# Performance work log

Measured on AMD Instinct MI355X. Metric: run time of the kernel, lower is better.

The kernel has to match this reference:

```python
import jax, jax.numpy as jnp
import numpy as np

B, C, H, W = 8192, 3, 32, 32
IN_FEATURES = C * H * W  # 3072, hardcoded in the module


def setup_inputs() -> dict:
    key = jax.random.key(0)
    k1, k2 = jax.random.split(key)
    x = jax.random.normal(k1, (B, C, H, W), dtype=jnp.float32)
    noise = jax.random.normal(k2, (B, C, H, W), dtype=jnp.float32)  # randn_like(x)
    logvar_t = jnp.array([-1.0], dtype=jnp.float32)  # nn.Parameter init
    return {"x": x, "noise": noise, "logvar_t": logvar_t}


def reference(x, noise, logvar_t):
    # additive branch of view_learner.forward
    n_batch = x.shape[0]
    x_t = x + jnp.exp(0.5 * logvar_t[0]) * noise
    var = jnp.exp(logvar_t[0]) + 1e-10
    xf = x.reshape(n_batch, IN_FEATURES)
    # compute_distances: x_norm + x_t_norm - 2 * x @ x.T, clamped to [0, inf)
    x_norm = jnp.sum(xf * xf, axis=1)  # [B]
    dist = x_norm[:, None] + x_norm[None, :] - 2.0 * (xf @ xf.T)  # [B, B]
    dist = jnp.maximum(dist, 0.0)
    distance_contribution = -jnp.mean(jax.nn.logsumexp(-0.5 * dist / var, axis=1))
    normalization_constant = jnp.log(jnp.float32(n_batch))
    kl_xt = (normalization_constant + distance_contribution) / jnp.log(jnp.float32(2.0))
    return x_t, kl_xt
```

## Files before the change

### kernel.cpp

```cpp
#include <hip/hip_runtime.h>
#include <cstdint>

#define K_DIM 3072
#define B_DIM 8192
#define ROW_B 3072
#define ROW_U 768
#define BMA   256
#define BNB   128
#define NTB   64
#define NKT   48

typedef __attribute__((ext_vector_type(4))) float        f32x4;
typedef __attribute__((ext_vector_type(4))) int          i32x4;

#define QS     16.0f
#define INV_S2 0.00390625f

__device__ __forceinline__ int q8(float f) {
    int q = __float2int_rn(f * QS);
    return max(-127, min(127, q));
}
__device__ __forceinline__ unsigned pack4(float a, float b, float c, float d) {
    return (unsigned)(q8(a) & 0xFF)
         | ((unsigned)(q8(b) & 0xFF) << 8)
         | ((unsigned)(q8(c) & 0xFF) << 16)
         | ((unsigned)(q8(d) & 0xFF) << 24);
}

__global__ __launch_bounds__(384) void prep_kernel(const float* __restrict__ x,
                                                   const float* __restrict__ nz,
                                                   const float* __restrict__ logvar,
                                                   float* __restrict__ xt,
                                                   unsigned int* __restrict__ xb,
                                                   float* __restrict__ xn,
                                                   float* __restrict__ se)
{
    const int row = blockIdx.x;
    const int tid = threadIdx.x;
    const float4* xr = (const float4*)(x + (size_t)row * K_DIM);
    float4 v0 = xr[2 * tid];
    float4 v1 = xr[2 * tid + 1];
    float s = v0.x * v0.x + v0.y * v0.y + v0.z * v0.z + v0.w * v0.w
            + v1.x * v1.x + v1.y * v1.y + v1.z * v1.z + v1.w * v1.w;

    if (xt) {
        const float4* nr = (const float4*)(nz + (size_t)row * K_DIM);
        float4 n0 = nr[2 * tid], n1 = nr[2 * tid + 1];
        const float sc = __expf(0.5f * logvar[0]);
        float4 o0, o1;
        o0.x = fmaf(sc, n0.x, v0.x); o0.y = fmaf(sc, n0.y, v0.y);
        o0.z = fmaf(sc, n0.z, v0.z); o0.w = fmaf(sc, n0.w, v0.w);
        o1.x = fmaf(sc, n1.x, v1.x); o1.y = fmaf(sc, n1.y, v1.y);
        o1.z = fmaf(sc, n1.z, v1.z); o1.w = fmaf(sc, n1.w, v1.w);
        float4* tr = (float4*)(xt + (size_t)row * K_DIM);
        tr[2 * tid] = o0;
        tr[2 * tid + 1] = o1;
    }

    unsigned int* dst = xb + (size_t)row * ROW_U + tid * 2;
    dst[0] = pack4(v0.x, v0.y, v0.z, v0.w);
    dst[1] = pack4(v1.x, v1.y, v1.z, v1.w);

#pragma unroll
    for (int d = 32; d > 0; d >>= 1) s += __shfl_down(s, d);
    __shared__ float red[6];
    if ((tid & 63) == 0) red[tid >> 6] = s;
    __syncthreads();
    if (tid == 0) {
        float t = 0.f;
#pragma unroll
        for (int i = 0; i < 6; ++i) t += red[i];
        xn[row] = t;
        se[row] = 0.f;
    }
}

__global__ __launch_bounds__(512, 4) void gram_lse_kernel(const unsigned int* __restrict__ xb,
                                                          const float* __restrict__ xn,
                                                          const float* __restrict__ logvar,
                                                          float* __restrict__ se)
{
    __shared__ __align__(1024) unsigned char lds[3][24576];

    int rem = blockIdx.x;
    int a = 0;
    while (rem >= NTB - 2 * a) { rem -= NTB - 2 * a; ++a; }
    const int v = 2 * a + rem;

    const int tid  = threadIdx.x;
    const int lane = tid & 63;
    const int wave = tid >> 6;
    const int wr = wave >> 1, wc = wave & 1;
    const int fc = lane >> 4;

    const size_t rowA0 = (size_t)a * BMA;
    const size_t rowB0 = (size_t)v * BNB;
    const unsigned char* xb8 = (const unsigned char*)xb;

    unsigned int srcOff[3];
    int dstOff[3];
#pragma unroll
    for (int l = 0; l < 3; ++l) {
        const int e = (l < 2) ? (l * 512 + tid) : tid;
        const int r = e >> 2, c = e & 3;
        const int csw = c ^ ((r >> 1) & 3);
        const size_t rb = ((l < 2) ? rowA0 : rowB0) + (size_t)r;
        srcOff[l] = (unsigned int)(rb * ROW_B + (size_t)csw * 16);
        dstOff[l] = ((l < 2) ? 0 : 16384) + e * 16;
    }

    i32x4 acc[4][4];
#pragma unroll
    for (int i = 0; i < 4; ++i)
#pragma unroll
        for (int j = 0; j < 4; ++j) acc[i][j] = (i32x4){0, 0, 0, 0};

#pragma unroll
    for (int l = 0; l < 3; ++l)
        __builtin_amdgcn_global_load_lds(
            (const __attribute__((address_space(1))) void*)(xb8 + srcOff[l]),
            (__attribute__((address_space(3))) void*)(&lds[0][0] + dstOff[l]), 16, 0, 0);
#pragma unroll
    for (int l = 0; l < 3; ++l)
        __builtin_amdgcn_global_load_lds(
            (const __attribute__((address_space(1))) void*)(xb8 + srcOff[l] + 64u),
            (__attribute__((address_space(3))) void*)(&lds[1][0] + dstOff[l]), 16, 0, 0);
    asm volatile("s_waitcnt vmcnt(3)" ::: "memory");
    asm volatile("s_barrier" ::: "memory");

    for (int t = 0; t < NKT; ++t) {
        const unsigned char* cur = &lds[t % 3][0];

        if (t + 2 < NKT) {
            unsigned char* nxt = &lds[(t + 2) % 3][0];
            const unsigned int kg = (unsigned int)(t + 2) * 64u;
#pragma unroll
            for (int l = 0; l < 3; ++l)
                __builtin_amdgcn_global_load_lds(
                    (const __attribute__((address_space(1))) void*)(xb8 + srcOff[l] + kg),
                    (__attribute__((address_space(3))) void*)(nxt + dstOff[l]), 16, 0, 0);
        }

        i32x4 aF[4], bF[4];
#pragma unroll
        for (int mi = 0; mi < 4; ++mi) {
            const int r = wr * 64 + mi * 16 + (lane & 15);
            const int phys = fc ^ ((r >> 1) & 3);
            aF[mi] = *(const i32x4*)(cur + r * 64 + phys * 16);
        }
#pragma unroll
        for (int ni = 0; ni < 4; ++ni) {
            const int r = wc * 64 + ni * 16 + (lane & 15);
            const int phys = fc ^ ((r >> 1) & 3);
            bF[ni] = *(const i32x4*)(cur + 16384 + r * 64 + phys * 16);
        }

        __builtin_amdgcn_s_setprio(1);
#pragma unroll
        for (int mi = 0; mi < 4; ++mi)
#pragma unroll
            for (int ni = 0; ni < 4; ++ni)
                acc[mi][ni] = __builtin_amdgcn_mfma_i32_16x16x64_i8(
                    aF[mi], bF[ni], acc[mi][ni], 0, 0, 0);
        __builtin_amdgcn_s_setprio(0);

        if (t + 2 < NKT)
            asm volatile("s_waitcnt vmcnt(3)" ::: "memory");
        else
            asm volatile("s_waitcnt vmcnt(0)" ::: "memory");
        asm volatile("s_barrier" ::: "memory");
    }

    const float lv  = logvar[0];
    const float var = __expf(lv) + 1e-10f;
    const float cc  = 0.5f / var;

    const int u = 2 * a + (wr >> 1);
    if (u > v) return;

    const int colBase = (int)rowB0 + wc * 64 + (lane & 15);
    const int rowBase = (int)rowA0 + wr * 64 + (lane >> 4) * 4;

#pragma unroll
    for (int mi = 0; mi < 4; ++mi) {
#pragma unroll
        for (int rg = 0; rg < 4; ++rg) {
            const int i = rowBase + mi * 16 + rg;
            const float xni = xn[i];
            float rs = 0.f;
#pragma unroll
            for (int ni = 0; ni < 4; ++ni) {
                const int j = colBase + ni * 16;
                const float g = (float)acc[mi][ni][rg] * INV_S2;
                const float dist = xni + xn[j] - 2.f * g;
                rs += (i == j) ? 1.0f : __expf(-cc * fmaxf(dist, 0.f));
            }
#pragma unroll
            for (int d = 1; d < 16; d <<= 1) rs += __shfl_xor(rs, d);
            if ((lane & 15) == 0) atomicAdd(&se[i], rs);
        }
    }

    if (u < v) {
#pragma unroll
        for (int ni = 0; ni < 4; ++ni) {
            const int j = colBase + ni * 16;
            const float xnj = xn[j];
            float cs = 0.f;
#pragma unroll
            for (int mi = 0; mi < 4; ++mi)
#pragma unroll
                for (int rg = 0; rg < 4; ++rg) {
                    const int i = rowBase + mi * 16 + rg;
                    const float g = (float)acc[mi][ni][rg] * INV_S2;
                    cs += __expf(-cc * fmaxf(xn[i] + xnj - 2.f * g, 0.f));
                }
#pragma unroll
            for (int d = 16; d < 64; d <<= 1) cs += __shfl_xor(cs, d);
            if ((lane >> 4) == 0) atomicAdd(&se[j], cs);
        }
    }
}

__global__ __launch_bounds__(256) void kl_kernel(const float* __restrict__ se,
                                                 float* __restrict__ out)
{
    const int tid = threadIdx.x;
    float s = 0.f;
    for (int i = tid; i < B_DIM; i += 256) s += logf(se[i]);
#pragma unroll
    for (int d = 32; d > 0; d >>= 1) s += __shfl_down(s, d);
    __shared__ float red[4];
    if ((tid & 63) == 0) red[tid >> 6] = s;
    __syncthreads();
    if (tid == 0) {
        const float dc = -(red[0] + red[1] + red[2] + red[3]) / (float)B_DIM;
        out[0] = (logf((float)B_DIM) + dc) / logf(2.f);
    }
}

__global__ __launch_bounds__(256) void xt_kernel(const float4* __restrict__ x,
                                                 const float4* __restrict__ nz,
                                                 const float* __restrict__ logvar,
                                                 float4* __restrict__ out, int n4)
{
    const float sc = expf(0.5f * logvar[0]);
    for (int i = blockIdx.x * blockDim.x + threadIdx.x; i < n4;
         i += gridDim.x * blockDim.x) {
        float4 va = x[i], vb = nz[i];
        float4 o;
        o.x = fmaf(sc, vb.x, va.x);
        o.y = fmaf(sc, vb.y, va.y);
        o.z = fmaf(sc, vb.z, va.z);
        o.w = fmaf(sc, vb.w, va.w);
        out[i] = o;
    }
}

extern "C" void kernel_launch(void* const* d_in, const int* in_sizes, int n_in,
                              void* d_out, int out_size, void* d_ws, size_t ws_size,
                              hipStream_t stream)
{
    const float* x      = (const float*)d_in[0];
    const float* noise  = (const float*)d_in[1];
    const float* logvar = (const float*)d_in[2];
    float* out = (float*)d_out;

    const size_t NEL      = (size_t)B_DIM * K_DIM;
    const size_t XB_BYTES = (size_t)B_DIM * ROW_B;
    const size_t NTILES   = 1056;

    const bool use_ws = ws_size >= XB_BYTES + 2 * (size_t)B_DIM * sizeof(float) + 256;

    if (use_ws) {
        unsigned int* xb = (unsigned int*)d_ws;
        float* xn = (float*)((char*)d_ws + XB_BYTES);
        float* se = xn + B_DIM;

        prep_kernel<<<B_DIM, 384, 0, stream>>>(x, noise, logvar, out, xb, xn, se);
        gram_lse_kernel<<<(int)NTILES, 512, 0, stream>>>(xb, xn, logvar, se);
        kl_kernel<<<1, 256, 0, stream>>>(se, out + NEL);
    } else {
        unsigned int* xb = (unsigned int*)d_out;
        float* xn = (float*)((char*)d_out + (32u << 20));
        float* se = xn + B_DIM;

        prep_kernel<<<B_DIM, 384, 0, stream>>>(x, noise, logvar, nullptr, xb, xn, se);
        gram_lse_kernel<<<(int)NTILES, 512, 0, stream>>>(xb, xn, logvar, se);
        kl_kernel<<<1, 256, 0, stream>>>(se, out + NEL);
        xt_kernel<<<2048, 256, 0, stream>>>((const float4*)x, (const float4*)noise,
                                            logvar, (float4*)out, (int)(NEL / 4));
    }
}
```

Before: 210.3 us.

## Use square 128x128 triangular tiles and double-buffer register fragments across k-steps

```diff
diff --git a/kernel.cpp b/kernel.cpp
--- a/kernel.cpp
+++ b/kernel.cpp
@@ -5,13 +5,12 @@
 #define B_DIM 8192
 #define ROW_B 3072
 #define ROW_U 768
-#define BMA   256
-#define BNB   128
-#define NTB   64
+#define BT    128
+#define NTT   64
 #define NKT   48
 
-typedef __attribute__((ext_vector_type(4))) float        f32x4;
-typedef __attribute__((ext_vector_type(4))) int          i32x4;
+typedef __attribute__((ext_vector_type(4))) float f32x4;
+typedef __attribute__((ext_vector_type(4))) int   i32x4;
 
 #define QS     16.0f
 #define INV_S2 0.00390625f
@@ -75,17 +74,19 @@
     }
 }
 
-__global__ __launch_bounds__(512, 4) void gram_lse_kernel(const unsigned int* __restrict__ xb,
+struct Frags { i32x4 a[4]; i32x4 b[4]; };
+
+__global__ __launch_bounds__(256, 3) void gram_lse_kernel(const unsigned int* __restrict__ xb,
                                                           const float* __restrict__ xn,
                                                           const float* __restrict__ logvar,
                                                           float* __restrict__ se)
 {
-    __shared__ __align__(1024) unsigned char lds[3][24576];
+    __shared__ __align__(1024) unsigned char lds[3][16384];
 
     int rem = blockIdx.x;
-    int a = 0;
-    while (rem >= NTB - 2 * a) { rem -= NTB - 2 * a; ++a; }
-    const int v = 2 * a + rem;
+    int bm = 0;
+    while (rem >= NTT - bm) { rem -= NTT - bm; ++bm; }
+    const int bn = bm + rem;
 
     const int tid  = threadIdx.x;
     const int lane = tid & 63;
@@ -93,20 +94,20 @@
     const int wr = wave >> 1, wc = wave & 1;
     const int fc = lane >> 4;
 
-    const size_t rowA0 = (size_t)a * BMA;
-    const size_t rowB0 = (size_t)v * BNB;
+    const size_t rowA0 = (size_t)bm * BT;
+    const size_t rowB0 = (size_t)bn * BT;
     const unsigned char* xb8 = (const unsigned char*)xb;
 
-    unsigned int srcOff[3];
-    int dstOff[3];
-#pragma unroll
-    for (int l = 0; l < 3; ++l) {
-        const int e = (l < 2) ? (l * 512 + tid) : tid;
+    unsigned int srcOff[4];
+    int dstOff[4];
+#pragma unroll
+    for (int l = 0; l < 4; ++l) {
+        const int e = (l & 1) * 256 + tid;
         const int r = e >> 2, c = e & 3;
         const int csw = c ^ ((r >> 1) & 3);
         const size_t rb = ((l < 2) ? rowA0 : rowB0) + (size_t)r;
         srcOff[l] = (unsigned int)(rb * ROW_B + (size_t)csw * 16);
-        dstOff[l] = ((l < 2) ? 0 : 16384) + e * 16;
+        dstOff[l] = ((l < 2) ? 0 : 8192) + e * 16;
     }
 
     i32x4 acc[4][4];
@@ -115,68 +116,78 @@
 #pragma unroll
         for (int j = 0; j < 4; ++j) acc[i][j] = (i32x4){0, 0, 0, 0};
 
-#pragma unroll
-    for (int l = 0; l < 3; ++l)
+    int aOff[4], bOff[4];
+#pragma unroll
+    for (int mi = 0; mi < 4; ++mi) {
+        const int r = wr * 64 + mi * 16 + (lane & 15);
+        aOff[mi] = r * 64 + (fc ^ ((r >> 1) & 3)) * 16;
+    }
+#pragma unroll
+    for (int ni = 0; ni < 4; ++ni) {
+        const int r = wc * 64 + ni * 16 + (lane & 15);
+        bOff[ni] = 8192 + r * 64 + (fc ^ ((r >> 1) & 3)) * 16;
+    }
+
+#pragma unroll
+    for (int l = 0; l < 4; ++l)
         __builtin_amdgcn_global_load_lds(
             (const __attribute__((address_space(1))) void*)(xb8 + srcOff[l]),
             (__attribute__((address_space(3))) void*)(&lds[0][0] + dstOff[l]), 16, 0, 0);
 #pragma unroll
-    for (int l = 0; l < 3; ++l)
+    for (int l = 0; l < 4; ++l)
         __builtin_amdgcn_global_load_lds(
             (const __attribute__((address_space(1))) void*)(xb8 + srcOff[l] + 64u),
             (__attribute__((address_space(3))) void*)(&lds[1][0] + dstOff[l]), 16, 0, 0);
-    asm volatile("s_waitcnt vmcnt(3)" ::: "memory");
+    asm volatile("s_waitcnt vmcnt(4)" ::: "memory");
     asm volatile("s_barrier" ::: "memory");
 
-    for (int t = 0; t < NKT; ++t) {
-        const unsigned char* cur = &lds[t % 3][0];
-
+    Frags fA, fB;
+#pragma unroll
+    for (int mi = 0; mi < 4; ++mi) fA.a[mi] = *(const i32x4*)(&lds[0][0] + aOff[mi]);
+#pragma unroll
+    for (int ni = 0; ni < 4; ++ni) fA.b[ni] = *(const i32x4*)(&lds[0][0] + bOff[ni]);
+
+    auto body = [&](int t, Frags& cur, Frags& nxt) {
         if (t + 2 < NKT) {
-            unsigned char* nxt = &lds[(t + 2) % 3][0];
+            unsigned char* buf = &lds[(t + 2) % 3][0];
             const unsigned int kg = (unsigned int)(t + 2) * 64u;
 #pragma unroll
-            for (int l = 0; l < 3; ++l)
+            for (int l = 0; l < 4; ++l)
                 __builtin_amdgcn_global_load_lds(
                     (const __attribute__((address_space(1))) void*)(xb8 + srcOff[l] + kg),
-                    (__attribute__((address_space(3))) void*)(nxt + dstOff[l]), 16, 0, 0);
+                    (__attribute__((address_space(3))) void*)(buf + dstOff[l]), 16, 0, 0);
         }
-
-        i32x4 aF[4], bF[4];
-#pragma unroll
-        for (int mi = 0; mi < 4; ++mi) {
-            const int r = wr * 64 + mi * 16 + (lane & 15);
-            const int phys = fc ^ ((r >> 1) & 3);
-            aF[mi] = *(const i32x4*)(cur + r * 64 + phys * 16);
-        }
-#pragma unroll
-        for (int ni = 0; ni < 4; ++ni) {
-            const int r = wc * 64 + ni * 16 + (lane & 15);
-            const int phys = fc ^ ((r >> 1) & 3);
-            bF[ni] = *(const i32x4*)(cur + 16384 + r * 64 + phys * 16);
-        }
-
-        __builtin_amdgcn_s_setprio(1);
-#pragma unroll
-        for (int mi = 0; mi < 4; ++mi)
-#pragma unroll
-            for (int ni = 0; ni < 4; ++ni)
-                acc[mi][ni] = __builtin_amdgcn_mfma_i32_16x16x64_i8(
-                    aF[mi], bF[ni], acc[mi][ni], 0, 0, 0);
-        __builtin_amdgcn_s_setprio(0);
-
+        asm volatile("s_waitcnt lgkmcnt(0)" ::: "memory");
         if (t + 2 < NKT)
-            asm volatile("s_waitcnt vmcnt(3)" ::: "memory");
+            asm volatile("s_waitcnt vmcnt(4)" ::: "memory");
         else
             asm volatile("s_waitcnt vmcnt(0)" ::: "memory");
         asm volatile("s_barrier" ::: "memory");
+        if (t + 1 < NKT) {
+            const unsigned char* buf = &lds[(t + 1) % 3][0];
+#pragma unroll
+            for (int mi = 0; mi < 4; ++mi) nxt.a[mi] = *(const i32x4*)(buf + aOff[mi]);
+#pragma unroll
+            for (int ni = 0; ni < 4; ++ni) nxt.b[ni] = *(const i32x4*)(buf + bOff[ni]);
+        }
+        __builtin_amdgcn_s_setprio(1);
+#pragma unroll
+        for (int mi = 0; mi < 4; ++mi)
+#pragma unroll
+            for (int ni = 0; ni < 4; ++ni)
+                acc[mi][ni] = __builtin_amdgcn_mfma_i32_16x16x64_i8(
+                    cur.a[mi], cur.b[ni], acc[mi][ni], 0, 0, 0);
+        __builtin_amdgcn_s_setprio(0);
+    };
+
+    for (int tt = 0; tt < NKT / 2; ++tt) {
+        body(2 * tt,     fA, fB);
+        body(2 * tt + 1, fB, fA);
     }
 
     const float lv  = logvar[0];
     const float var = __expf(lv) + 1e-10f;
     const float cc  = 0.5f / var;
-
-    const int u = 2 * a + (wr >> 1);
-    if (u > v) return;
 
     const int colBase = (int)rowB0 + wc * 64 + (lane & 15);
     const int rowBase = (int)rowA0 + wr * 64 + (lane >> 4) * 4;
@@ -201,7 +212,7 @@
         }
     }
 
-    if (u < v) {
+    if (bm != bn) {
 #pragma unroll
         for (int ni = 0; ni < 4; ++ni) {
             const int j = colBase + ni * 16;
@@ -268,7 +279,7 @@
 
     const size_t NEL      = (size_t)B_DIM * K_DIM;
     const size_t XB_BYTES = (size_t)B_DIM * ROW_B;
-    const size_t NTILES   = 1056;
+    const int    NTILES   = NTT * (NTT + 1) / 2;
 
     const bool use_ws = ws_size >= XB_BYTES + 2 * (size_t)B_DIM * sizeof(float) + 256;
 
@@ -278,7 +289,7 @@
         float* se = xn + B_DIM;
 
         prep_kernel<<<B_DIM, 384, 0, stream>>>(x, noise, logvar, out, xb, xn, se);
-        gram_lse_kernel<<<(int)NTILES, 512, 0, stream>>>(xb, xn, logvar, se);
+        gram_lse_kernel<<<NTILES, 256, 0, stream>>>(xb, xn, logvar, se);
         kl_kernel<<<1, 256, 0, stream>>>(se, out + NEL);
     } else {
         unsigned int* xb = (unsigned int*)d_out;
@@ -286,7 +297,7 @@
         float* se = xn + B_DIM;
 
         prep_kernel<<<B_DIM, 384, 0, stream>>>(x, noise, logvar, nullptr, xb, xn, se);
-        gram_lse_kernel<<<(int)NTILES, 512, 0, stream>>>(xb, xn, logvar, se);
+        gram_lse_kernel<<<NTILES, 256, 0, stream>>>(xb, xn, logvar, se);
         kl_kernel<<<1, 256, 0, stream>>>(se, out + NEL);
         xt_kernel<<<2048, 256, 0, stream>>>((const float4*)x, (const float4*)noise,
                                             logvar, (float4*)out, (int)(NEL / 4));
```

Result: slower. 225.9 us (+7.4%).

## Double K-tile depth, interleave prefetch with MFMA phases, swizzle block order

Applied to the files above, without the earlier changes.

```diff
diff --git a/kernel.cpp b/kernel.cpp
--- a/kernel.cpp
+++ b/kernel.cpp
@@ -8,10 +8,12 @@
 #define BMA   256
 #define BNB   128
 #define NTB   64
-#define NKT   48
-
-typedef __attribute__((ext_vector_type(4))) float        f32x4;
-typedef __attribute__((ext_vector_type(4))) int          i32x4;
+#define NKT   24
+#define ABYTES 32768
+#define BUFSZ  49152
+
+typedef __attribute__((ext_vector_type(4))) float f32x4;
+typedef __attribute__((ext_vector_type(4))) int   i32x4;
 
 #define QS     16.0f
 #define INV_S2 0.00390625f
@@ -75,14 +77,15 @@
     }
 }
 
-__global__ __launch_bounds__(512, 4) void gram_lse_kernel(const unsigned int* __restrict__ xb,
+__global__ __launch_bounds__(512, 1) void gram_lse_kernel(const unsigned int* __restrict__ xb,
                                                           const float* __restrict__ xn,
                                                           const float* __restrict__ logvar,
                                                           float* __restrict__ se)
 {
-    __shared__ __align__(1024) unsigned char lds[3][24576];
-
-    int rem = blockIdx.x;
+    __shared__ __align__(1024) unsigned char lds[3][BUFSZ];
+
+    const int orig = blockIdx.x;
+    int rem = (orig & 7) * 132 + (orig >> 3);
     int a = 0;
     while (rem >= NTB - 2 * a) { rem -= NTB - 2 * a; ++a; }
     const int v = 2 * a + rem;
@@ -97,16 +100,32 @@
     const size_t rowB0 = (size_t)v * BNB;
     const unsigned char* xb8 = (const unsigned char*)xb;
 
-    unsigned int srcOff[3];
-    int dstOff[3];
-#pragma unroll
-    for (int l = 0; l < 3; ++l) {
-        const int e = (l < 2) ? (l * 512 + tid) : tid;
-        const int r = e >> 2, c = e & 3;
-        const int csw = c ^ ((r >> 1) & 3);
-        const size_t rb = ((l < 2) ? rowA0 : rowB0) + (size_t)r;
+    unsigned int srcOff[6];
+    int dstOff[6];
+#pragma unroll
+    for (int l = 0; l < 6; ++l) {
+        const int e = (l < 4) ? (l * 512 + tid) : ((l - 4) * 512 + tid);
+        const int r = e >> 3, c = e & 7;
+        const int csw = c ^ (r & 7);
+        const size_t rb = ((l < 4) ? rowA0 : rowB0) + (size_t)r;
         srcOff[l] = (unsigned int)(rb * ROW_B + (size_t)csw * 16);
-        dstOff[l] = ((l < 2) ? 0 : 16384) + e * 16;
+        dstOff[l] = ((l < 4) ? 0 : ABYTES) + e * 16;
+    }
+
+    int aOff[4][2], bOff[4][2];
+#pragma unroll
+    for (int mi = 0; mi < 4; ++mi) {
+        const int r = wr * 64 + mi * 16 + (lane & 15);
+#pragma unroll
+        for (int kp = 0; kp < 2; ++kp)
+            aOff[mi][kp] = r * 128 + ((kp * 4 + fc) ^ (r & 7)) * 16;
+    }
+#pragma unroll
+    for (int ni = 0; ni < 4; ++ni) {
+        const int r = wc * 64 + ni * 16 + (lane & 15);
+#pragma unroll
+        for (int kp = 0; kp < 2; ++kp)
+            bOff[ni][kp] = ABYTES + r * 128 + ((kp * 4 + fc) ^ (r & 7)) * 16;
     }
 
     i32x4 acc[4][4];
@@ -115,61 +134,86 @@
 #pragma unroll
         for (int j = 0; j < 4; ++j) acc[i][j] = (i32x4){0, 0, 0, 0};
 
-#pragma unroll
-    for (int l = 0; l < 3; ++l)
-        __builtin_amdgcn_global_load_lds(
-            (const __attribute__((address_space(1))) void*)(xb8 + srcOff[l]),
-            (__attribute__((address_space(3))) void*)(&lds[0][0] + dstOff[l]), 16, 0, 0);
-#pragma unroll
-    for (int l = 0; l < 3; ++l)
-        __builtin_amdgcn_global_load_lds(
-            (const __attribute__((address_space(1))) void*)(xb8 + srcOff[l] + 64u),
-            (__attribute__((address_space(3))) void*)(&lds[1][0] + dstOff[l]), 16, 0, 0);
-    asm volatile("s_waitcnt vmcnt(3)" ::: "memory");
+#define GLOAD(l, t, buf)                                                          \
+    __builtin_amdgcn_global_load_lds(                                             \
+        (const __attribute__((address_space(1))) void*)(xb8 + srcOff[l] + (unsigned)(t) * 128u), \
+        (__attribute__((address_space(3))) void*)(&lds[buf][0] + dstOff[l]), 16, 0, 0)
+
+#pragma unroll
+    for (int l = 0; l < 6; ++l) GLOAD(l, 0, 0);
+#pragma unroll
+    for (int l = 0; l < 6; ++l) GLOAD(l, 1, 1);
+    asm volatile("s_waitcnt vmcnt(6)" ::: "memory");
     asm volatile("s_barrier" ::: "memory");
 
     for (int t = 0; t < NKT; ++t) {
         const unsigned char* cur = &lds[t % 3][0];
-
-        if (t + 2 < NKT) {
-            unsigned char* nxt = &lds[(t + 2) % 3][0];
-            const unsigned int kg = (unsigned int)(t + 2) * 64u;
-#pragma unroll
-            for (int l = 0; l < 3; ++l)
-                __builtin_amdgcn_global_load_lds(
-                    (const __attribute__((address_space(1))) void*)(xb8 + srcOff[l] + kg),
-                    (__attribute__((address_space(3))) void*)(nxt + dstOff[l]), 16, 0, 0);
-        }
-
-        i32x4 aF[4], bF[4];
-#pragma unroll
-        for (int mi = 0; mi < 4; ++mi) {
-            const int r = wr * 64 + mi * 16 + (lane & 15);
-            const int phys = fc ^ ((r >> 1) & 3);
-            aF[mi] = *(const i32x4*)(cur + r * 64 + phys * 16);
-        }
-#pragma unroll
-        for (int ni = 0; ni < 4; ++ni) {
-            const int r = wc * 64 + ni * 16 + (lane & 15);
-            const int phys = fc ^ ((r >> 1) & 3);
-            bF[ni] = *(const i32x4*)(cur + 16384 + r * 64 + phys * 16);
-        }
-
+        const int nb = (t + 2) % 3;
+        const bool pf = (t + 2 < NKT);
+
+        i32x4 aF0, aF1, bF[4];
+
+        aF0 = *(const i32x4*)(cur + aOff[0][0]);
+        aF1 = *(const i32x4*)(cur + aOff[1][0]);
+#pragma unroll
+        for (int ni = 0; ni < 4; ++ni) bF[ni] = *(const i32x4*)(cur + bOff[ni][0]);
+        if (pf) { GLOAD(0, t + 2, nb); GLOAD(1, t + 2, nb); }
+        asm volatile("s_barrier" ::: "memory");
         __builtin_amdgcn_s_setprio(1);
 #pragma unroll
-        for (int mi = 0; mi < 4; ++mi)
-#pragma unroll
-            for (int ni = 0; ni < 4; ++ni)
-                acc[mi][ni] = __builtin_amdgcn_mfma_i32_16x16x64_i8(
-                    aF[mi], bF[ni], acc[mi][ni], 0, 0, 0);
+        for (int ni = 0; ni < 4; ++ni) {
+            acc[0][ni] = __builtin_amdgcn_mfma_i32_16x16x64_i8(aF0, bF[ni], acc[0][ni], 0, 0, 0);
+            acc[1][ni] = __builtin_amdgcn_mfma_i32_16x16x64_i8(aF1, bF[ni], acc[1][ni], 0, 0, 0);
+        }
         __builtin_amdgcn_s_setprio(0);
-
-        if (t + 2 < NKT)
-            asm volatile("s_waitcnt vmcnt(3)" ::: "memory");
+        asm volatile("s_barrier" ::: "memory");
+
+        aF0 = *(const i32x4*)(cur + aOff[2][0]);
+        aF1 = *(const i32x4*)(cur + aOff[3][0]);
+        if (pf) { GLOAD(2, t + 2, nb); GLOAD(3, t + 2, nb); }
+        asm volatile("s_barrier" ::: "memory");
+        __builtin_amdgcn_s_setprio(1);
+#pragma unroll
+        for (int ni = 0; ni < 4; ++ni) {
+            acc[2][ni] = __builtin_amdgcn_mfma_i32_16x16x64_i8(aF0, bF[ni], acc[2][ni], 0, 0, 0);
+            acc[3][ni] = __builtin_amdgcn_mfma_i32_16x16x64_i8(aF1, bF[ni], acc[3][ni], 0, 0, 0);
+        }
+        __builtin_amdgcn_s_setprio(0);
+        asm volatile("s_barrier" ::: "memory");
+
+        aF0 = *(const i32x4*)(cur + aOff[0][1]);
+        aF1 = *(const i32x4*)(cur + aOff[1][1]);
+#pragma unroll
+        for (int ni = 0; ni < 4; ++ni) bF[ni] = *(const i32x4*)(cur + bOff[ni][1]);
+        if (pf) GLOAD(4, t + 2, nb);
+        asm volatile("s_barrier" ::: "memory");
+        __builtin_amdgcn_s_setprio(1);
+#pragma unroll
+        for (int ni = 0; ni < 4; ++ni) {
+            acc[0][ni] = __builtin_amdgcn_mfma_i32_16x16x64_i8(aF0, bF[ni], acc[0][ni], 0, 0, 0);
+            acc[1][ni] = __builtin_amdgcn_mfma_i32_16x16x64_i8(aF1, bF[ni], acc[1][ni], 0, 0, 0);
+        }
+        __builtin_amdgcn_s_setprio(0);
+        asm volatile("s_barrier" ::: "memory");
+
+        aF0 = *(const i32x4*)(cur + aOff[2][1]);
+        aF1 = *(const i32x4*)(cur + aOff[3][1]);
+        if (pf) GLOAD(5, t + 2, nb);
+        asm volatile("s_barrier" ::: "memory");
+        __builtin_amdgcn_s_setprio(1);
+#pragma unroll
+        for (int ni = 0; ni < 4; ++ni) {
+            acc[2][ni] = __builtin_amdgcn_mfma_i32_16x16x64_i8(aF0, bF[ni], acc[2][ni], 0, 0, 0);
+            acc[3][ni] = __builtin_amdgcn_mfma_i32_16x16x64_i8(aF1, bF[ni], acc[3][ni], 0, 0, 0);
+        }
+        __builtin_amdgcn_s_setprio(0);
+        if (pf)
+            asm volatile("s_waitcnt vmcnt(6)" ::: "memory");
         else
             asm volatile("s_waitcnt vmcnt(0)" ::: "memory");
         asm volatile("s_barrier" ::: "memory");
     }
+#undef GLOAD
 
     const float lv  = logvar[0];
     const float var = __expf(lv) + 1e-10f;
@@ -268,7 +312,7 @@
 
     const size_t NEL      = (size_t)B_DIM * K_DIM;
     const size_t XB_BYTES = (size_t)B_DIM * ROW_B;
-    const size_t NTILES   = 1056;
+    const int    NTILES   = 1056;
 
     const bool use_ws = ws_size >= XB_BYTES + 2 * (size_t)B_DIM * sizeof(float) + 256;
 
@@ -278,7 +322,7 @@
         float* se = xn + B_DIM;
 
         prep_kernel<<<B_DIM, 384, 0, stream>>>(x, noise, logvar, out, xb, xn, se);
-        gram_lse_kernel<<<(int)NTILES, 512, 0, stream>>>(xb, xn, logvar, se);
+        gram_lse_kernel<<<NTILES, 512, 0, stream>>>(xb, xn, logvar, se);
         kl_kernel<<<1, 256, 0, stream>>>(se, out + NEL);
     } else {
         unsigned int* xb = (unsigned int*)d_out;
@@ -286,7 +330,7 @@
         float* se = xn + B_DIM;
 
         prep_kernel<<<B_DIM, 384, 0, stream>>>(x, noise, logvar, nullptr, xb, xn, se);
-        gram_lse_kernel<<<(int)NTILES, 512, 0, stream>>>(xb, xn, logvar, se);
+        gram_lse_kernel<<<NTILES, 512, 0, stream>>>(xb, xn, logvar, se);
         kl_kernel<<<1, 256, 0, stream>>>(se, out + NEL);
         xt_kernel<<<2048, 256, 0, stream>>>((const float4*)x, (const float4*)noise,
                                             logvar, (float4*)out, (int)(NEL / 4));
```

Result: slower. 242.3 us (+15.2%).

## Move x_t elementwise computation from prep kernel into gram kernel tail

Applied to the files above, without the earlier changes.

```diff
diff --git a/kernel.cpp b/kernel.cpp
--- a/kernel.cpp
+++ b/kernel.cpp
@@ -9,6 +9,8 @@
 #define BNB   128
 #define NTB   64
 #define NKT   48
+#define NTILES 1056
+#define N4     6291456
 
 typedef __attribute__((ext_vector_type(4))) float        f32x4;
 typedef __attribute__((ext_vector_type(4))) int          i32x4;
@@ -28,9 +30,6 @@
 }
 
 __global__ __launch_bounds__(384) void prep_kernel(const float* __restrict__ x,
-                                                   const float* __restrict__ nz,
-                                                   const float* __restrict__ logvar,
-                                                   float* __restrict__ xt,
                                                    unsigned int* __restrict__ xb,
                                                    float* __restrict__ xn,
                                                    float* __restrict__ se)
@@ -43,20 +42,6 @@
     float s = v0.x * v0.x + v0.y * v0.y + v0.z * v0.z + v0.w * v0.w
             + v1.x * v1.x + v1.y * v1.y + v1.z * v1.z + v1.w * v1.w;
 
-    if (xt) {
-        const float4* nr = (const float4*)(nz + (size_t)row * K_DIM);
-        float4 n0 = nr[2 * tid], n1 = nr[2 * tid + 1];
-        const float sc = __expf(0.5f * logvar[0]);
-        float4 o0, o1;
-        o0.x = fmaf(sc, n0.x, v0.x); o0.y = fmaf(sc, n0.y, v0.y);
-        o0.z = fmaf(sc, n0.z, v0.z); o0.w = fmaf(sc, n0.w, v0.w);
-        o1.x = fmaf(sc, n1.x, v1.x); o1.y = fmaf(sc, n1.y, v1.y);
-        o1.z = fmaf(sc, n1.z, v1.z); o1.w = fmaf(sc, n1.w, v1.w);
-        float4* tr = (float4*)(xt + (size_t)row * K_DIM);
-        tr[2 * tid] = o0;
-        tr[2 * tid + 1] = o1;
-    }
-
     unsigned int* dst = xb + (size_t)row * ROW_U + tid * 2;
     dst[0] = pack4(v0.x, v0.y, v0.z, v0.w);
     dst[1] = pack4(v1.x, v1.y, v1.z, v1.w);
@@ -78,7 +63,10 @@
 __global__ __launch_bounds__(512, 4) void gram_lse_kernel(const unsigned int* __restrict__ xb,
                                                           const float* __restrict__ xn,
                                                           const float* __restrict__ logvar,
-                                                          float* __restrict__ se)
+                                                          float* __restrict__ se,
+                                                          const float4* __restrict__ x4,
+                                                          const float4* __restrict__ nz4,
+                                                          float4* __restrict__ xt4)
 {
     __shared__ __align__(1024) unsigned char lds[3][24576];
 
@@ -172,6 +160,20 @@
     }
 
     const float lv  = logvar[0];
+
+    if (xt4) {
+        const float sc = __expf(0.5f * lv);
+        for (int i = blockIdx.x * 512 + tid; i < N4; i += NTILES * 512) {
+            float4 va = x4[i], vb = nz4[i];
+            float4 o;
+            o.x = fmaf(sc, vb.x, va.x);
+            o.y = fmaf(sc, vb.y, va.y);
+            o.z = fmaf(sc, vb.z, va.z);
+            o.w = fmaf(sc, vb.w, va.w);
+            xt4[i] = o;
+        }
+    }
+
     const float var = __expf(lv) + 1e-10f;
     const float cc  = 0.5f / var;
 
@@ -268,7 +270,6 @@
 
     const size_t NEL      = (size_t)B_DIM * K_DIM;
     const size_t XB_BYTES = (size_t)B_DIM * ROW_B;
-    const size_t NTILES   = 1056;
 
     const bool use_ws = ws_size >= XB_BYTES + 2 * (size_t)B_DIM * sizeof(float) + 256;
 
@@ -277,16 +278,22 @@
         float* xn = (float*)((char*)d_ws + XB_BYTES);
         float* se = xn + B_DIM;
 
-        prep_kernel<<<B_DIM, 384, 0, stream>>>(x, noise, logvar, out, xb, xn, se);
-        gram_lse_kernel<<<(int)NTILES, 512, 0, stream>>>(xb, xn, logvar, se);
+        prep_kernel<<<B_DIM, 384, 0, stream>>>(x, xb, xn, se);
+        gram_lse_kernel<<<NTILES, 512, 0, stream>>>(xb, xn, logvar, se,
+                                                    (const float4*)x,
+                                                    (const float4*)noise,
+                                                    (float4*)out);
         kl_kernel<<<1, 256, 0, stream>>>(se, out + NEL);
     } else {
         unsigned int* xb = (unsigned int*)d_out;
         float* xn = (float*)((char*)d_out + (32u << 20));
         float* se = xn + B_DIM;
 
-        prep_kernel<<<B_DIM, 384, 0, stream>>>(x, noise, logvar, nullptr, xb, xn, se);
-        gram_lse_kernel<<<(int)NTILES, 512, 0, stream>>>(xb, xn, logvar, se);
+        prep_kernel<<<B_DIM, 384, 0, stream>>>(x, xb, xn, se);
+        gram_lse_kernel<<<NTILES, 512, 0, stream>>>(xb, xn, logvar, se,
+                                                    (const float4*)x,
+                                                    (const float4*)noise,
+                                                    nullptr);
         kl_kernel<<<1, 256, 0, stream>>>(se, out + NEL);
         xt_kernel<<<2048, 256, 0, stream>>>((const float4*)x, (const float4*)noise,
                                             logvar, (float4*)out, (int)(NEL / 4));
```

New measurement: 210.5 us. Within noise of the previous version (+0.1%).
